# Kernel tuning notes

Measured on AMD Instinct MI355X. Metric: run time of the kernel, lower is better.

The kernel has to match this reference:

```python
import jax, jax.numpy as jnp
import numpy as np

B, S, DIM = 2, 2048, 2048
H = 16
Q_LORA, KV_LORA = 512, 512
D_NOPE, D_ROPE, D_V = 128, 64, 128
D_QK = D_NOPE + D_ROPE  # 192
SCALE = D_QK ** -0.5
EPS = 1e-6


def rmsnorm(x, w):
    return x * jax.lax.rsqrt(jnp.mean(x * x, axis=-1, keepdims=True) + EPS) * w


def apply_rope(x, cos, sin):
    # x: [B, S, h, d] with d even; cos/sin: [S, d//2] (complex-pair rotation)
    xs = x.reshape(*x.shape[:-1], -1, 2)
    x0, x1 = xs[..., 0], xs[..., 1]
    c = cos[None, :, None, :]
    s = sin[None, :, None, :]
    out = jnp.stack([x0 * c - x1 * s, x0 * s + x1 * c], axis=-1)
    return out.reshape(x.shape)


def setup_inputs() -> dict:
    key = jax.random.key(0)
    ks = jax.random.split(key, 8)
    std = 0.02
    x = jax.random.normal(ks[0], (B, S, DIM), dtype=jnp.float32)
    wq_a_w = jax.random.normal(ks[1], (DIM, Q_LORA), dtype=jnp.float32) * std
    wq_a_b = jnp.zeros((Q_LORA,), dtype=jnp.float32)
    q_norm_w = jnp.ones((Q_LORA,), dtype=jnp.float32)
    wq_b_w = jax.random.normal(ks[2], (Q_LORA, H * D_QK), dtype=jnp.float32) * std
    wkv_a_w = jax.random.normal(ks[3], (DIM, KV_LORA + D_ROPE), dtype=jnp.float32) * std
    wkv_a_b = jnp.zeros((KV_LORA + D_ROPE,), dtype=jnp.float32)
    kv_norm_w = jnp.ones((KV_LORA,), dtype=jnp.float32)
    wkv_b_w = jax.random.normal(ks[4], (KV_LORA, H * (D_NOPE + D_V)), dtype=jnp.float32) * std
    wo_w = jax.random.normal(ks[5], (H * D_V, DIM), dtype=jnp.float32) * std
    # rotary table: freqs_cis[t, i] = exp(1j * t * 10000^{-2i/d})
    inv_freq = 1.0 / (10000.0 ** (np.arange(0, D_ROPE, 2, dtype=np.float32) / D_ROPE))
    t = np.arange(S, dtype=np.float32)
    ang = np.outer(t, inv_freq)  # [S, D_ROPE//2]
    freqs_cos = jnp.asarray(np.cos(ang), dtype=jnp.float32)
    freqs_sin = jnp.asarray(np.sin(ang), dtype=jnp.float32)
    # causal mask (prefill): 0 on/below diagonal, -1e9 above
    mask = jnp.where(jnp.arange(S)[:, None] >= jnp.arange(S)[None, :], 0.0, -1e9).astype(jnp.float32)
    return {"x": x, "wq_a_w": wq_a_w, "wq_a_b": wq_a_b, "q_norm_w": q_norm_w,
            "wq_b_w": wq_b_w, "wkv_a_w": wkv_a_w, "wkv_a_b": wkv_a_b,
            "kv_norm_w": kv_norm_w, "wkv_b_w": wkv_b_w, "wo_w": wo_w,
            "freqs_cos": freqs_cos, "freqs_sin": freqs_sin, "mask": mask,
            "start_pos": 0}


def reference(x, wq_a_w, wq_a_b, q_norm_w, wq_b_w, wkv_a_w, wkv_a_b,
              kv_norm_w, wkv_b_w, wo_w, freqs_cos, freqs_sin, mask, start_pos):
    bsz, seqlen, _ = x.shape
    # low-rank Q: wq_b(q_norm(wq_a(x)))
    q = rmsnorm(x @ wq_a_w + wq_a_b, q_norm_w) @ wq_b_w
    q = q.reshape(bsz, seqlen, H, D_QK)
    q_nope, q_pe = q[..., :D_NOPE], q[..., D_NOPE:]
    q_pe = apply_rope(q_pe, freqs_cos, freqs_sin)
    # low-rank KV
    kv_full = x @ wkv_a_w + wkv_a_b
    kv, k_pe = kv_full[..., :KV_LORA], kv_full[..., KV_LORA:]
    k_pe = apply_rope(k_pe[:, :, None, :], freqs_cos, freqs_sin)  # [B,S,1,D_ROPE]
    kv = rmsnorm(kv, kv_norm_w) @ wkv_b_w
    kv = kv.reshape(bsz, seqlen, H, D_NOPE + D_V)
    k_nope, v = kv[..., :D_NOPE], kv[..., D_NOPE:]
    k = jnp.concatenate([k_nope, jnp.broadcast_to(k_pe, (bsz, seqlen, H, D_ROPE))], axis=-1)
    # prefill (start_pos=0): cache[:, :end_pos] == freshly written k, v
    q = jnp.concatenate([q_nope, q_pe], axis=-1)
    scores = jnp.einsum('bshd,bthd->bsht', q, k) * SCALE
    scores = scores + mask[None, :, None, :]
    attn = jax.nn.softmax(scores.astype(jnp.float32), axis=-1).astype(q.dtype)
    out = jnp.einsum('bsht,bthd->bshd', attn, v)
    return out.reshape(bsz, seqlen, H * D_V) @ wo_w
```

## Files before the change

### kernel.cpp

```cpp
#include <hip/hip_runtime.h>
#include <hip/hip_bf16.h>

typedef unsigned short u16;
typedef unsigned int u32;
typedef __attribute__((ext_vector_type(8))) __bf16 bf16x8;
typedef __attribute__((ext_vector_type(4))) float f32x4;
typedef __attribute__((ext_vector_type(4))) u32 u32x4;
typedef __attribute__((ext_vector_type(2))) u32 u32x2;

#define S_LEN 2048
#define BF16_ONE 0x3F80u

__device__ __forceinline__ float b2f(u16 u) {
  union { unsigned u; float f; } v; v.u = ((unsigned)u) << 16; return v.f;
}
__device__ __forceinline__ u16 f2b(float f) {
  union { float f; unsigned u; } v; v.f = f;
  unsigned r = v.u + 0x7fffu + ((v.u >> 16) & 1u);
  return (u16)(r >> 16);
}
__device__ __forceinline__ u32 cvt_pk_bf16(float a, float b) {
  u32 r;
  asm("v_cvt_pk_bf16_f32 %0, %1, %2" : "=v"(r) : "v"(a), "v"(b));
  return r;
}

__device__ __forceinline__ void glds16(const u16* g, u16* l) {
  __builtin_amdgcn_global_load_lds((const __attribute__((address_space(1))) void*)g,
                                   (__attribute__((address_space(3))) void*)l, 16, 0, 0);
}

__device__ __forceinline__ bool probe_f32(const u16* p) { return p[0] != (u16)BF16_ONE; }

struct CvtDesc {
  const void* src[7];
  u16* dst[7];
  int cum[8];
};
struct TrDesc {
  const void* in[5];
  u16* out[5];
  int R[5], C[5];
  int tcum[6];
  float scale[5];
};

__global__ __launch_bounds__(256) void prep_all(CvtDesc d, TrDesc td,
                                                const u16* __restrict__ probe,
                                                int cvt_total, int cvt_blocks) {
  const int tid = threadIdx.x;
  if ((int)blockIdx.x < cvt_blocks) {
    int i = blockIdx.x * 256 + tid;
    if (i >= cvt_total) return;
    int t = 0;
#pragma unroll
    for (int k = 1; k < 7; ++k) t += (i >= d.cum[k]);
    int li = i - d.cum[t];
    if (probe_f32(probe)) {
      const float* s = (const float*)d.src[t] + (long)li * 8;
      u16 tmp[8];
#pragma unroll
      for (int j = 0; j < 8; ++j) tmp[j] = f2b(s[j]);
      *(u32x4*)(d.dst[t] + (long)li * 8) = *(const u32x4*)tmp;
    } else {
      *(u32x4*)(d.dst[t] + (long)li * 8) = ((const u32x4*)d.src[t])[li];
    }
  } else {
    __shared__ u16 tile[32][33];
    int bid = blockIdx.x - cvt_blocks;
    int t = 0;
#pragma unroll
    for (int k = 1; k < 5; ++k) t += (bid >= td.tcum[k]);
    int rem = bid - td.tcum[t];
    const int R = td.R[t], C = td.C[t];
    const int tilesX = C >> 5;
    const int bx = rem % tilesX, by = rem / tilesX;
    const int c0 = bx * 32, r0 = by * 32;
    const int tx = tid & 31, ty = tid >> 5;
    const float sc = td.scale[t];
    if (probe_f32(probe)) {
      const float* inf = (const float*)td.in[t];
#pragma unroll
      for (int i = 0; i < 4; ++i)
        tile[ty + i * 8][tx] = f2b(inf[(long)(r0 + ty + i * 8) * C + c0 + tx] * sc);
    } else {
      const u16* inb = (const u16*)td.in[t];
#pragma unroll
      for (int i = 0; i < 4; ++i)
        tile[ty + i * 8][tx] = f2b(b2f(inb[(long)(r0 + ty + i * 8) * C + c0 + tx]) * sc);
    }
    __syncthreads();
    u16* outp = td.out[t];
#pragma unroll
    for (int i = 0; i < 4; ++i)
      outp[(long)(c0 + ty + i * 8) * R + r0 + tx] = tile[tx][ty + i * 8];
  }
}

template <int MT>
__global__ __launch_bounds__(256) void gemm_bt(const u16* __restrict__ A,
                                               const u16* __restrict__ Bt,
                                               const u16* __restrict__ bias,
                                               void* __restrict__ Cv,
                                               int M, int N, int K,
                                               const u16* __restrict__ oprobe,
                                               u16* __restrict__ vtOut) {
  constexpr int MI = MT / 32;
  __shared__ u16 As[2][MT * 32];
  __shared__ u16 Bs[2][128 * 32];
  const int tid = threadIdx.x;
  const int lane = tid & 63;
  const int w = tid >> 6;
  const int quad = lane >> 4;
  const int l16 = lane & 15;
  const int m0 = blockIdx.y * MT;
  const int n0 = blockIdx.x * 128;
  const int wm = (w >> 1) * (MT / 2);
  const int wn = (w & 1) * 64;

  const f32x4 zero = {0.f, 0.f, 0.f, 0.f};
  f32x4 acc[MI][4];
#pragma unroll
  for (int i = 0; i < MI; ++i)
#pragma unroll
    for (int j = 0; j < 4; ++j) acc[i][j] = zero;

  auto stage = [&](int k0, int buf) {
#pragma unroll
    for (int cc = 0; cc < MT * 4; cc += 256) {
      int j = cc + tid, ar = j >> 2, ak = ((j & 3) ^ (ar & 3)) * 8;
      glds16(A + (long)(m0 + ar) * K + k0 + ak, As[buf] + j * 8);
    }
#pragma unroll
    for (int cc = 0; cc < 512; cc += 256) {
      int j = cc + tid, br = j >> 2, bk = ((j & 3) ^ (br & 3)) * 8;
      int bn = n0 + br; if (bn > N - 1) bn = N - 1;
      glds16(Bt + (long)bn * K + k0 + bk, Bs[buf] + j * 8);
    }
  };

  const int nk = K >> 5;
  stage(0, 0);
  for (int t = 0; t < nk; ++t) {
    __syncthreads();
    if (t + 1 < nk) stage((t + 1) << 5, (t + 1) & 1);
    const u16* as = As[t & 1];
    const u16* bs = Bs[t & 1];
    bf16x8 af[MI], bfr[4];
#pragma unroll
    for (int mi = 0; mi < MI; ++mi)
      af[mi] = *(const bf16x8*)(as + (wm + mi * 16 + l16) * 32 +
                                ((quad ^ (l16 & 3)) * 8));
#pragma unroll
    for (int ni = 0; ni < 4; ++ni)
      bfr[ni] = *(const bf16x8*)(bs + (wn + ni * 16 + l16) * 32 +
                                 ((quad ^ (l16 & 3)) * 8));
#pragma unroll
    for (int mi = 0; mi < MI; ++mi)
#pragma unroll
      for (int ni = 0; ni < 4; ++ni)
        acc[mi][ni] = __builtin_amdgcn_mfma_f32_16x16x32_bf16(af[mi], bfr[ni],
                                                              acc[mi][ni], 0, 0, 0);
  }

  u16* C = (u16*)Cv;
  float* Cf = (float*)Cv;
  const bool of32 = oprobe && probe_f32(oprobe);
#pragma unroll
  for (int ni = 0; ni < 4; ++ni) {
    int col = n0 + wn + ni * 16 + l16;
    if (col >= N) continue;
    float bv = bias ? b2f(bias[col]) : 0.0f;
    const int lc = col & 255;
    const bool toV = (vtOut != nullptr) && (lc >= 128);
#pragma unroll
    for (int mi = 0; mi < MI; ++mi) {
      int row = m0 + wm + mi * 16 + quad * 4;
      if (toV) {
        int hh = col >> 8, d = lc - 128;
        int bb = row >> 11, s = row & 2047;
        u32 lo = (u32)f2b(acc[mi][ni][0] + bv) | ((u32)f2b(acc[mi][ni][1] + bv) << 16);
        u32 hi = (u32)f2b(acc[mi][ni][2] + bv) | ((u32)f2b(acc[mi][ni][3] + bv) << 16);
        u32x2 pk = {lo, hi};
        *(u32x2*)(vtOut + ((long)(bb * 16 + hh) * 128 + d) * 2048 + s) = pk;
      } else {
#pragma unroll
        for (int r = 0; r < 4; ++r) {
          float val = acc[mi][ni][r] + bv;
          if (of32) Cf[(long)(row + r) * N + col] = val;
          else      C[(long)(row + r) * N + col] = f2b(val);
        }
      }
    }
  }
}

__global__ __launch_bounds__(256) void gemm_qkv(const u16* __restrict__ qa,
                                                const u16* __restrict__ wqbT,
                                                u16* __restrict__ qbuf,
                                                const u16* __restrict__ kvn,
                                                const u16* __restrict__ wkvbT,
                                                u16* __restrict__ kvb,
                                                u16* __restrict__ vtb) {
  constexpr int MT = 128, MI = 4, K = 512;
  __shared__ u16 As[2][MT * 32];
  __shared__ u16 Bs[2][128 * 32];
  const bool isQ = blockIdx.x < 24;
  const u16* A  = isQ ? qa : kvn;
  const u16* Bt = isQ ? wqbT : wkvbT;
  u16* C        = isQ ? qbuf : kvb;
  u16* vtOut    = isQ ? (u16*)nullptr : vtb;
  const int N   = isQ ? 3072 : 4096;
  const int bx  = isQ ? (int)blockIdx.x : (int)blockIdx.x - 24;
  const int tid = threadIdx.x;
  const int lane = tid & 63;
  const int w = tid >> 6;
  const int quad = lane >> 4;
  const int l16 = lane & 15;
  const int m0 = blockIdx.y * MT;
  const int n0 = bx * 128;
  const int wm = (w >> 1) * (MT / 2);
  const int wn = (w & 1) * 64;

  const f32x4 zero = {0.f, 0.f, 0.f, 0.f};
  f32x4 acc[MI][4];
#pragma unroll
  for (int i = 0; i < MI; ++i)
#pragma unroll
    for (int j = 0; j < 4; ++j) acc[i][j] = zero;

  auto stage = [&](int k0, int buf) {
#pragma unroll
    for (int cc = 0; cc < MT * 4; cc += 256) {
      int j = cc + tid, ar = j >> 2, ak = ((j & 3) ^ (ar & 3)) * 8;
      glds16(A + (long)(m0 + ar) * K + k0 + ak, As[buf] + j * 8);
    }
#pragma unroll
    for (int cc = 0; cc < 512; cc += 256) {
      int j = cc + tid, br = j >> 2, bk = ((j & 3) ^ (br & 3)) * 8;
      glds16(Bt + (long)(n0 + br) * K + k0 + bk, Bs[buf] + j * 8);
    }
  };

  const int nk = K >> 5;
  stage(0, 0);
  for (int t = 0; t < nk; ++t) {
    __syncthreads();
    if (t + 1 < nk) stage((t + 1) << 5, (t + 1) & 1);
    const u16* as = As[t & 1];
    const u16* bs = Bs[t & 1];
    bf16x8 af[MI], bfr[4];
#pragma unroll
    for (int mi = 0; mi < MI; ++mi)
      af[mi] = *(const bf16x8*)(as + (wm + mi * 16 + l16) * 32 +
                                ((quad ^ (l16 & 3)) * 8));
#pragma unroll
    for (int ni = 0; ni < 4; ++ni)
      bfr[ni] = *(const bf16x8*)(bs + (wn + ni * 16 + l16) * 32 +
                                 ((quad ^ (l16 & 3)) * 8));
#pragma unroll
    for (int mi = 0; mi < MI; ++mi)
#pragma unroll
      for (int ni = 0; ni < 4; ++ni)
        acc[mi][ni] = __builtin_amdgcn_mfma_f32_16x16x32_bf16(af[mi], bfr[ni],
                                                              acc[mi][ni], 0, 0, 0);
  }

#pragma unroll
  for (int ni = 0; ni < 4; ++ni) {
    int col = n0 + wn + ni * 16 + l16;
    const int lc = col & 255;
    const bool toV = (vtOut != nullptr) && (lc >= 128);
#pragma unroll
    for (int mi = 0; mi < MI; ++mi) {
      int row = m0 + wm + mi * 16 + quad * 4;
      if (toV) {
        int hh = col >> 8, d = lc - 128;
        int bb = row >> 11, s = row & 2047;
        u32 lo = (u32)f2b(acc[mi][ni][0]) | ((u32)f2b(acc[mi][ni][1]) << 16);
        u32 hi = (u32)f2b(acc[mi][ni][2]) | ((u32)f2b(acc[mi][ni][3]) << 16);
        u32x2 pk = {lo, hi};
        *(u32x2*)(vtOut + ((long)(bb * 16 + hh) * 128 + d) * 2048 + s) = pk;
      } else {
#pragma unroll
        for (int r = 0; r < 4; ++r)
          C[(long)(row + r) * N + col] = f2b(acc[mi][ni][r]);
      }
    }
  }
}

__global__ __launch_bounds__(256) void rmsnorm_dual(const u16* __restrict__ qkva,
                                                    const u16* __restrict__ qw,
                                                    const u16* __restrict__ kw,
                                                    u16* __restrict__ qa,
                                                    u16* __restrict__ kvn) {
  __shared__ float red[4];
  const int bid = blockIdx.x;
  const bool kv = bid >= 4096;
  const int row = kv ? bid - 4096 : bid;
  const int tid = threadIdx.x;
  const u16* x = qkva + (long)row * 1088 + (kv ? 512 : 0);
  const u16* w = kv ? kw : qw;
  u16* y = (kv ? kvn : qa) + (long)row * 512;
  float v0 = b2f(x[tid]), v1 = b2f(x[tid + 256]);
  float ss = v0 * v0 + v1 * v1;
#pragma unroll
  for (int off = 1; off < 64; off <<= 1) ss += __shfl_xor(ss, off);
  if ((tid & 63) == 0) red[tid >> 6] = ss;
  __syncthreads();
  float tot = red[0] + red[1] + red[2] + red[3];
  float r = rsqrtf(tot * (1.0f / 512.0f) + 1e-6f);
  y[tid] = f2b(v0 * r * b2f(w[tid]));
  y[tid + 256] = f2b(v1 * r * b2f(w[tid + 256]));
}

__global__ __launch_bounds__(256) void rope_all(u16* __restrict__ q,
                                                const u16* __restrict__ qkva,
                                                u16* __restrict__ kpe,
                                                const u16* __restrict__ fc,
                                                const u16* __restrict__ fs) {
  const int bid = blockIdx.x;
  if (bid < 8192) {
    int i = bid * 256 + threadIdx.x;
    int pair = i & 31;
    int h = (i >> 5) & 15;
    int row = i >> 9;
    int pos = row & (S_LEN - 1);
    long base = (long)row * 3072 + h * 192 + 128 + pair * 2;
    float x0 = b2f(q[base]), x1 = b2f(q[base + 1]);
    float c = b2f(fc[pos * 32 + pair]), s = b2f(fs[pos * 32 + pair]);
    q[base] = f2b(x0 * c - x1 * s);
    q[base + 1] = f2b(x0 * s + x1 * c);
  } else {
    int i = (bid - 8192) * 256 + threadIdx.x;
    int pair = i & 31;
    int row = i >> 5;
    int pos = row & (S_LEN - 1);
    long sb = (long)row * 1088 + 1024 + pair * 2;
    float x0 = b2f(qkva[sb]), x1 = b2f(qkva[sb + 1]);
    float c = b2f(fc[pos * 32 + pair]), s = b2f(fs[pos * 32 + pair]);
    kpe[(long)row * 64 + pair * 2] = f2b(x0 * c - x1 * s);
    kpe[(long)row * 64 + pair * 2 + 1] = f2b(x0 * s + x1 * c);
  }
}

__global__ __launch_bounds__(512, 1) void mla_attn(const u16* __restrict__ q,
                                                   const u16* __restrict__ kvb,
                                                   const u16* __restrict__ vt,
                                                   const u16* __restrict__ kpe,
                                                   u16* __restrict__ o) {
  __shared__ u16 Ks[2][2][64 * 192];
  __shared__ u16 Vts[2][128 * 64];
  const int tid = threadIdx.x;
  const int w = tid >> 6;
  const int g = w >> 2;
  const int sw = w & 3;
  const int lane = tid & 63;
  const int quad = lane >> 4;
  const int l16 = lane & 15;
  const int bh = blockIdx.x;
  const int b = bh >> 4, h = bh & 15;
  const long rowbase = (long)b * S_LEN;
  const f32x4 zero = {0.f, 0.f, 0.f, 0.f};

  auto stage_k = [&](int t0s, u16* dst) {
#pragma unroll
    for (int tt = 0; tt < 3; ++tt) {
      int j = tt * 512 + tid;
      int r = j / 24, csw = j % 24;
      int c = csw ^ (r & 7);
      const u16* src = (c < 16)
                           ? (kvb + (rowbase + t0s + r) * 4096 + h * 256 + c * 8)
                           : (kpe + (rowbase + t0s + r) * 64 + (c - 16) * 8);
      glds16(src, dst + j * 8);
    }
  };
  auto stage_v = [&](int t0s, u16* dst) {
#pragma unroll
    for (int tt = 0; tt < 2; ++tt) {
      int j = tt * 512 + tid;
      int d = j >> 3, c = (j & 7) ^ (d & 7);
      glds16(vt + ((long)bh * 128 + d) * S_LEN + t0s + c * 8, dst + j * 8);
    }
  };

  const int srcA = (((quad & 1) << 1) | (quad >> 1)) * 16 + l16;
  const int srcB = srcA ^ 16;
  const bool lowq = quad < 2;
  const int p = quad & 1;

  const int yy = blockIdx.y;
  const int jt = (yy < 8) ? yy : 23 - yy;
  const int q0 = jt * 128;
  const int ns = jt + 1;
  const int rowlo = q0 + sw * 32;

  const u16* qrowA = q + (rowbase + rowlo + l16) * 3072 + h * 192;
  const u16* qrowB = qrowA + 16 * 3072;
  bf16x8 qfA[6], qfB[6];
#pragma unroll
  for (int kk = 0; kk < 6; ++kk) {
    qfA[kk] = *(const bf16x8*)(qrowA + kk * 32 + quad * 8);
    qfB[kk] = *(const bf16x8*)(qrowB + kk * 32 + quad * 8);
  }

  float mA = -INFINITY, mB = -INFINITY;
  float lA = 0.f, lB = 0.f;
  f32x4 oA[8], oB[8];
#pragma unroll
  for (int i = 0; i < 8; ++i) { oA[i] = zero; oB[i] = zero; }

  auto finish_half = [&](f32x4* s, float& m_r, float& l_r, f32x4* oacc,
                         int lim, bool needmask, bf16x8& ap0, bf16x8& ap1) {
    if (needmask) {
#pragma unroll
      for (int gg = 0; gg < 4; ++gg)
#pragma unroll
        for (int r = 0; r < 4; ++r)
          s[gg][r] = (gg * 16 + r > lim) ? -1e30f : s[gg][r];
    }
    float mx0 = fmaxf(fmaxf(s[0][0], s[0][1]), fmaxf(s[0][2], s[0][3]));
    float mx1 = fmaxf(fmaxf(s[1][0], s[1][1]), fmaxf(s[1][2], s[1][3]));
    float mx2 = fmaxf(fmaxf(s[2][0], s[2][1]), fmaxf(s[2][2], s[2][3]));
    float mx3 = fmaxf(fmaxf(s[3][0], s[3][1]), fmaxf(s[3][2], s[3][3]));
    float vmax = fmaxf(fmaxf(mx0, mx1), fmaxf(mx2, mx3));
    vmax = fmaxf(vmax, __shfl_xor(vmax, 16));
    vmax = fmaxf(vmax, __shfl_xor(vmax, 32));

    if (!__all(vmax <= m_r + 8.0f)) {
      float mnew = fmaxf(m_r, vmax);
      float alpha = __expf(m_r - mnew);
      m_r = mnew;
      l_r *= alpha;
      float al0 = __shfl(alpha, (lane & 48) | (quad * 4 + 0));
      float al1 = __shfl(alpha, (lane & 48) | (quad * 4 + 1));
      float al2 = __shfl(alpha, (lane & 48) | (quad * 4 + 2));
      float al3 = __shfl(alpha, (lane & 48) | (quad * 4 + 3));
#pragma unroll
      for (int nt = 0; nt < 8; ++nt) {
        f32x4 tt = oacc[nt];
        tt[0] *= al0; tt[1] *= al1; tt[2] *= al2; tt[3] *= al3;
        oacc[nt] = tt;
      }
    }

    float e00 = __expf(s[0][0] - m_r), e01 = __expf(s[0][1] - m_r);
    float e02 = __expf(s[0][2] - m_r), e03 = __expf(s[0][3] - m_r);
    float e10 = __expf(s[1][0] - m_r), e11 = __expf(s[1][1] - m_r);
    float e12 = __expf(s[1][2] - m_r), e13 = __expf(s[1][3] - m_r);
    float e20 = __expf(s[2][0] - m_r), e21 = __expf(s[2][1] - m_r);
    float e22 = __expf(s[2][2] - m_r), e23 = __expf(s[2][3] - m_r);
    float e30 = __expf(s[3][0] - m_r), e31 = __expf(s[3][1] - m_r);
    float e32 = __expf(s[3][2] - m_r), e33 = __expf(s[3][3] - m_r);
    l_r += ((e00 + e01) + (e02 + e03)) + ((e10 + e11) + (e12 + e13)) +
           ((e20 + e21) + (e22 + e23)) + ((e30 + e31) + (e32 + e33));
    u32 pk0x = cvt_pk_bf16(e00, e01), pk0y = cvt_pk_bf16(e02, e03);
    u32 pk1x = cvt_pk_bf16(e10, e11), pk1y = cvt_pk_bf16(e12, e13);
    u32 pk2x = cvt_pk_bf16(e20, e21), pk2y = cvt_pk_bf16(e22, e23);
    u32 pk3x = cvt_pk_bf16(e30, e31), pk3y = cvt_pk_bf16(e32, e33);

    u32 a0c = p ? pk1x : pk0x, a1c = p ? pk1y : pk0y;
    u32 a2c = p ? pk3x : pk2x, a3c = p ? pk3y : pk2y;
    u32 b0c = p ? pk0x : pk1x, b1c = p ? pk0y : pk1y;
    u32 b2c = p ? pk2x : pk3x, b3c = p ? pk2y : pk3y;
    u32 A0 = __shfl(a0c, srcA), A1 = __shfl(a1c, srcA);
    u32 A2 = __shfl(a2c, srcA), A3 = __shfl(a3c, srcA);
    u32 B0 = __shfl(b0c, srcB), B1 = __shfl(b1c, srcB);
    u32 B2 = __shfl(b2c, srcB), B3 = __shfl(b3c, srcB);
    u32x4 w0 = {lowq ? A0 : B0, lowq ? A1 : B1, lowq ? B0 : A0, lowq ? B1 : A1};
    u32x4 w1 = {lowq ? A2 : B2, lowq ? A3 : B3, lowq ? B2 : A2, lowq ? B3 : A3};
    ap0 = __builtin_bit_cast(bf16x8, w0);
    ap1 = __builtin_bit_cast(bf16x8, w1);
  };

  stage_k(0, Ks[0][0]);
  stage_k(64, Ks[0][1]);

  for (int i = 0; i < ns; ++i) {
    __syncthreads();
    stage_v((2 * i) * 64, Vts[0]);
    stage_v((2 * i + 1) * 64, Vts[1]);
    if (i + 1 < ns) {
      stage_k((2 * i + 2) * 64, Ks[(i + 1) & 1][0]);
      stage_k((2 * i + 3) * 64, Ks[(i + 1) & 1][1]);
    }
    const int t0 = (2 * i + g) * 64;
    const bool active = (rowlo + 31 >= t0);
    bf16x8 apA0, apA1, apB0, apB1;
    if (active) {
      const u16* ks = Ks[i & 1][g];
      f32x4 sA[4] = {zero, zero, zero, zero};
      f32x4 sB[4] = {zero, zero, zero, zero};
      __builtin_amdgcn_s_setprio(1);
#pragma unroll
      for (int kk = 0; kk < 6; ++kk) {
        const int csw = ((kk * 4 + quad) ^ (l16 & 7)) * 8;
#pragma unroll
        for (int gg = 0; gg < 4; ++gg) {
          bf16x8 kf = *(const bf16x8*)(ks + (gg * 16 + l16) * 192 + csw);
          sA[gg] = __builtin_amdgcn_mfma_f32_16x16x32_bf16(kf, qfA[kk], sA[gg], 0, 0, 0);
          sB[gg] = __builtin_amdgcn_mfma_f32_16x16x32_bf16(kf, qfB[kk], sB[gg], 0, 0, 0);
        }
      }
      __builtin_amdgcn_s_setprio(0);

      const bool nmA = (t0 + 63 > rowlo);
      const bool nmB = (t0 + 63 > rowlo + 16);
      const int limA = rowlo + l16 - t0 - quad * 4;
      finish_half(sA, mA, lA, oA, limA, nmA, apA0, apA1);
      finish_half(sB, mB, lB, oB, limA + 16, nmB, apB0, apB1);
    }
    __syncthreads();
    if (active) {
      const u16* vs = Vts[g];
      __builtin_amdgcn_s_setprio(1);
#pragma unroll
      for (int nt = 0; nt < 8; ++nt) {
        bf16x8 bv0 = *(const bf16x8*)(vs + (nt * 16 + l16) * 64 +
                                      ((quad ^ (l16 & 7)) * 8));
        bf16x8 bv1 = *(const bf16x8*)(vs + (nt * 16 + l16) * 64 +
                                      (((4 + quad) ^ (l16 & 7)) * 8));
        oA[nt] = __builtin_amdgcn_mfma_f32_16x16x32_bf16(apA0, bv0, oA[nt], 0, 0, 0);
        oA[nt] = __builtin_amdgcn_mfma_f32_16x16x32_bf16(apA1, bv1, oA[nt], 0, 0, 0);
        oB[nt] = __builtin_amdgcn_mfma_f32_16x16x32_bf16(apB0, bv0, oB[nt], 0, 0, 0);
        oB[nt] = __builtin_amdgcn_mfma_f32_16x16x32_bf16(apB1, bv1, oB[nt], 0, 0, 0);
      }
      __builtin_amdgcn_s_setprio(0);
    }
  }

  float lsA = lA; lsA += __shfl_xor(lsA, 16); lsA += __shfl_xor(lsA, 32);
  float lsB = lB; lsB += __shfl_xor(lsB, 16); lsB += __shfl_xor(lsB, 32);

  float* zone = (float*)&Ks[0][0][0];
  float* mlz = zone + 16384;
  if (g == 1) {
    float* zp0 = zone + ((sw * 2 + 0) * 64 + lane) * 32;
    float* zp1 = zone + ((sw * 2 + 1) * 64 + lane) * 32;
#pragma unroll
    for (int nt = 0; nt < 8; ++nt) {
      *(f32x4*)(zp0 + ((nt ^ (lane & 7)) << 2)) = oA[nt];
      *(f32x4*)(zp1 + ((nt ^ (lane & 7)) << 2)) = oB[nt];
    }
    mlz[((sw * 2 + 0) * 64 + lane) * 2 + 0] = mA;
    mlz[((sw * 2 + 0) * 64 + lane) * 2 + 1] = lsA;
    mlz[((sw * 2 + 1) * 64 + lane) * 2 + 0] = mB;
    mlz[((sw * 2 + 1) * 64 + lane) * 2 + 1] = lsB;
  }
  __syncthreads();
  if (g == 0) {
    auto merge_write = [&](float m_r, float ls, f32x4* oacc, int hz) {
      const float* zp = zone + ((sw * 2 + hz) * 64 + lane) * 32;
      float mo = mlz[((sw * 2 + hz) * 64 + lane) * 2 + 0];
      float lo = mlz[((sw * 2 + hz) * 64 + lane) * 2 + 1];
      float mm = fmaxf(m_r, mo);
      float aA = __expf(m_r - mm);
      float aB = __expf(mo - mm);
      float lt = ls * aA + lo * aB;
      float sAl = __fdividef(aA, lt);
      float sBl = __fdividef(aB, lt);
      float sa[4], sb[4];
#pragma unroll
      for (int r = 0; r < 4; ++r) {
        int src = (lane & 48) | (quad * 4 + r);
        sa[r] = __shfl(sAl, src);
        sb[r] = __shfl(sBl, src);
      }
      const long orow = rowbase + q0 + sw * 32 + hz * 16 + quad * 4;
#pragma unroll
      for (int nt = 0; nt < 8; ++nt) {
        f32x4 op = *(const f32x4*)(zp + ((nt ^ (lane & 7)) << 2));
#pragma unroll
        for (int r = 0; r < 4; ++r)
          o[(orow + r) * 2048 + h * 128 + nt * 16 + l16] =
              f2b(oacc[nt][r] * sa[r] + op[r] * sb[r]);
      }
    };
    merge_write(mA, lsA, oA, 0);
    merge_write(mB, lsB, oB, 1);
  }
}

extern "C" void kernel_launch(void* const* d_in, const int* in_sizes, int n_in,
                              void* d_out, int out_size, void* d_ws, size_t ws_size,
                              hipStream_t stream) {
  const void* x_raw    = d_in[0];
  const void* wqa_raw  = d_in[1];
  const void* wqab_raw = d_in[2];
  const void* qnw_raw  = d_in[3];
  const void* wqb_raw  = d_in[4];
  const void* wkva_raw = d_in[5];
  const void* wkvab_raw= d_in[6];
  const void* kvnw_raw = d_in[7];
  const void* wkvb_raw = d_in[8];
  const void* wo_raw   = d_in[9];
  const void* fc_raw   = d_in[10];
  const void* fs_raw   = d_in[11];
  const u16* probe = (const u16*)qnw_raw;
  const float SC = 0.07216878364870323f;

  char* ws = (char*)d_ws;
  size_t off = 0;
  auto alloc = [&](size_t n) { void* p = ws + off; off += (n + 255) & ~(size_t)255; return p; };
  u16* xb     = (u16*)alloc(4096ull * 2048 * 2);
  u16* fcb    = (u16*)alloc(2048ull * 32 * 2);
  u16* fsb    = (u16*)alloc(2048ull * 32 * 2);
  u16* biasc  = (u16*)alloc(1088ull * 2);
  u16* qnw_b  = (u16*)alloc(512ull * 2);
  u16* kvnw_b = (u16*)alloc(512ull * 2);
  u16* qkvat  = (u16*)alloc(1088ull * 2048 * 2);
  u16* wqb_t  = (u16*)alloc(3072ull * 512 * 2);
  u16* wkvb_t = (u16*)alloc(4096ull * 512 * 2);
  u16* wo_t   = (u16*)alloc(2048ull * 2048 * 2);
  u16* qkva   = (u16*)alloc(4096ull * 1088 * 2);
  u16* qa     = (u16*)alloc(4096ull * 512 * 2);
  u16* qbuf   = (u16*)alloc(4096ull * 3072 * 2);
  u16* kvn    = (u16*)alloc(4096ull * 512 * 2);
  u16* kpe    = (u16*)alloc(4096ull * 64 * 2);
  u16* kvb    = (u16*)alloc(4096ull * 4096 * 2);
  u16* vtb    = (u16*)alloc(32ull * 128 * 2048 * 2);
  u16* attn   = (u16*)alloc(4096ull * 2048 * 2);

  CvtDesc cd;
  const void* csrc[7] = {x_raw, fc_raw, fs_raw, wqab_raw, qnw_raw, wkvab_raw, kvnw_raw};
  u16* cdst[7] = {xb, fcb, fsb, biasc, qnw_b, biasc + 512, kvnw_b};
  long cn[7] = {4096l * 2048, 2048l * 32, 2048l * 32, 512, 512, 576, 512};
  int cum = 0;
  for (int i = 0; i < 7; ++i) {
    cd.src[i] = csrc[i]; cd.dst[i] = cdst[i];
    cd.cum[i] = cum; cum += (int)(cn[i] / 8);
  }
  cd.cum[7] = cum;

  TrDesc td;
  const void* tin[5] = {wqa_raw, wqb_raw, wkva_raw, wkvb_raw, wo_raw};
  u16* tout[5] = {qkvat, wqb_t, qkvat + 512ull * 2048, wkvb_t, wo_t};
  int tR[5] = {2048, 512, 2048, 512, 2048};
  int tC[5] = {512, 3072, 576, 4096, 2048};
  float tsc[5] = {1.0f, SC, 1.0f, 1.0f, 1.0f};
  int tcum = 0;
  for (int i = 0; i < 5; ++i) {
    td.in[i] = tin[i]; td.out[i] = tout[i];
    td.R[i] = tR[i]; td.C[i] = tC[i]; td.scale[i] = tsc[i];
    td.tcum[i] = tcum; tcum += (tR[i] / 32) * (tC[i] / 32);
  }
  td.tcum[5] = tcum;

  int cvt_blocks = (cum + 255) / 256;
  prep_all<<<cvt_blocks + tcum, 256, 0, stream>>>(cd, td, probe, cum, cvt_blocks);

  gemm_bt<128><<<dim3(9, 32), 256, 0, stream>>>(xb, qkvat, biasc, qkva, 4096, 1088, 2048,
                                                nullptr, nullptr);

  rmsnorm_dual<<<8192, 256, 0, stream>>>(qkva, qnw_b, kvnw_b, qa, kvn);

  gemm_qkv<<<dim3(56, 32), 256, 0, stream>>>(qa, wqb_t, qbuf, kvn, wkvb_t, kvb, vtb);

  rope_all<<<8704, 256, 0, stream>>>(qbuf, qkva, kpe, fcb, fsb);

  mla_attn<<<dim3(32, 16), 512, 0, stream>>>(qbuf, kvb, vtb, kpe, attn);

  gemm_bt<128><<<dim3(16, 32), 256, 0, stream>>>(attn, wo_t, nullptr, d_out, 4096, 2048, 2048,
                                                 probe, nullptr);
}
```

Before: 376.5 us.

## Fuse k_pe rope into rmsnorm kernel and apply q rope inside attention

Removes the standalone rope kernel. The k_pe rotation now runs in extra blocks of the rmsnorm kernel, and the q_pe rotation is applied to the Q fragments after they are loaded into registers in the attention kernel. This drops one launch and a full read-modify-write pass over the q buffer, in exchange for a few extra global loads of cos/sin and some ALU work at the start of each attention block. The pair mapping per lane has to match the fragment layout exactly.

Measured after the change: 373.6 us. About the same (-0.8%).

```diff
diff --git a/kernel.cpp b/kernel.cpp
--- a/kernel.cpp
+++ b/kernel.cpp
@@ -290,50 +290,18 @@
   }
 }
 
-__global__ __launch_bounds__(256) void rmsnorm_dual(const u16* __restrict__ qkva,
+__global__ __launch_bounds__(256) void rmsnorm_rope(const u16* __restrict__ qkva,
                                                     const u16* __restrict__ qw,
                                                     const u16* __restrict__ kw,
                                                     u16* __restrict__ qa,
-                                                    u16* __restrict__ kvn) {
-  __shared__ float red[4];
+                                                    u16* __restrict__ kvn,
+                                                    u16* __restrict__ kpe,
+                                                    const u16* __restrict__ fc,
+                                                    const u16* __restrict__ fs) {
   const int bid = blockIdx.x;
-  const bool kv = bid >= 4096;
-  const int row = kv ? bid - 4096 : bid;
   const int tid = threadIdx.x;
-  const u16* x = qkva + (long)row * 1088 + (kv ? 512 : 0);
-  const u16* w = kv ? kw : qw;
-  u16* y = (kv ? kvn : qa) + (long)row * 512;
-  float v0 = b2f(x[tid]), v1 = b2f(x[tid + 256]);
-  float ss = v0 * v0 + v1 * v1;
-#pragma unroll
-  for (int off = 1; off < 64; off <<= 1) ss += __shfl_xor(ss, off);
-  if ((tid & 63) == 0) red[tid >> 6] = ss;
-  __syncthreads();
-  float tot = red[0] + red[1] + red[2] + red[3];
-  float r = rsqrtf(tot * (1.0f / 512.0f) + 1e-6f);
-  y[tid] = f2b(v0 * r * b2f(w[tid]));
-  y[tid + 256] = f2b(v1 * r * b2f(w[tid + 256]));
-}
-
-__global__ __launch_bounds__(256) void rope_all(u16* __restrict__ q,
-                                                const u16* __restrict__ qkva,
-                                                u16* __restrict__ kpe,
-                                                const u16* __restrict__ fc,
-                                                const u16* __restrict__ fs) {
-  const int bid = blockIdx.x;
-  if (bid < 8192) {
-    int i = bid * 256 + threadIdx.x;
-    int pair = i & 31;
-    int h = (i >> 5) & 15;
-    int row = i >> 9;
-    int pos = row & (S_LEN - 1);
-    long base = (long)row * 3072 + h * 192 + 128 + pair * 2;
-    float x0 = b2f(q[base]), x1 = b2f(q[base + 1]);
-    float c = b2f(fc[pos * 32 + pair]), s = b2f(fs[pos * 32 + pair]);
-    q[base] = f2b(x0 * c - x1 * s);
-    q[base + 1] = f2b(x0 * s + x1 * c);
-  } else {
-    int i = (bid - 8192) * 256 + threadIdx.x;
+  if (bid >= 8192) {
+    int i = (bid - 8192) * 256 + tid;
     int pair = i & 31;
     int row = i >> 5;
     int pos = row & (S_LEN - 1);
@@ -342,13 +310,32 @@
     float c = b2f(fc[pos * 32 + pair]), s = b2f(fs[pos * 32 + pair]);
     kpe[(long)row * 64 + pair * 2] = f2b(x0 * c - x1 * s);
     kpe[(long)row * 64 + pair * 2 + 1] = f2b(x0 * s + x1 * c);
-  }
+    return;
+  }
+  __shared__ float red[4];
+  const bool kv = bid >= 4096;
+  const int row = kv ? bid - 4096 : bid;
+  const u16* x = qkva + (long)row * 1088 + (kv ? 512 : 0);
+  const u16* w = kv ? kw : qw;
+  u16* y = (kv ? kvn : qa) + (long)row * 512;
+  float v0 = b2f(x[tid]), v1 = b2f(x[tid + 256]);
+  float ss = v0 * v0 + v1 * v1;
+#pragma unroll
+  for (int off = 1; off < 64; off <<= 1) ss += __shfl_xor(ss, off);
+  if ((tid & 63) == 0) red[tid >> 6] = ss;
+  __syncthreads();
+  float tot = red[0] + red[1] + red[2] + red[3];
+  float r = rsqrtf(tot * (1.0f / 512.0f) + 1e-6f);
+  y[tid] = f2b(v0 * r * b2f(w[tid]));
+  y[tid + 256] = f2b(v1 * r * b2f(w[tid + 256]));
 }
 
 __global__ __launch_bounds__(512, 1) void mla_attn(const u16* __restrict__ q,
                                                    const u16* __restrict__ kvb,
                                                    const u16* __restrict__ vt,
                                                    const u16* __restrict__ kpe,
+                                                   const u16* __restrict__ fc,
+                                                   const u16* __restrict__ fs,
                                                    u16* __restrict__ o) {
   __shared__ u16 Ks[2][2][64 * 192];
   __shared__ u16 Vts[2][128 * 64];
@@ -403,6 +390,23 @@
   for (int kk = 0; kk < 6; ++kk) {
     qfA[kk] = *(const bf16x8*)(qrowA + kk * 32 + quad * 8);
     qfB[kk] = *(const bf16x8*)(qrowB + kk * 32 + quad * 8);
+  }
+  auto rope_frag = [&](bf16x8& f, int pos, int pb) {
+    u32x4 v = __builtin_bit_cast(u32x4, f);
+#pragma unroll
+    for (int j = 0; j < 4; ++j) {
+      u32 wv = v[j];
+      float x0 = b2f((u16)(wv & 0xffff)), x1 = b2f((u16)(wv >> 16));
+      float c = b2f(fc[pos * 32 + pb + j]), s = b2f(fs[pos * 32 + pb + j]);
+      v[j] = (u32)f2b(x0 * c - x1 * s) | ((u32)f2b(x0 * s + x1 * c) << 16);
+    }
+    f = __builtin_bit_cast(bf16x8, v);
+  };
+#pragma unroll
+  for (int kk = 4; kk < 6; ++kk) {
+    const int pb = (kk - 4) * 16 + quad * 4;
+    rope_frag(qfA[kk], rowlo + l16, pb);
+    rope_frag(qfB[kk], rowlo + 16 + l16, pb);
   }
 
   float mA = -INFINITY, mB = -INFINITY;
@@ -653,13 +657,11 @@
   gemm_bt<128><<<dim3(9, 32), 256, 0, stream>>>(xb, qkvat, biasc, qkva, 4096, 1088, 2048,
                                                 nullptr, nullptr);
 
-  rmsnorm_dual<<<8192, 256, 0, stream>>>(qkva, qnw_b, kvnw_b, qa, kvn);
+  rmsnorm_rope<<<8704, 256, 0, stream>>>(qkva, qnw_b, kvnw_b, qa, kvn, kpe, fcb, fsb);
 
   gemm_qkv<<<dim3(56, 32), 256, 0, stream>>>(qa, wqb_t, qbuf, kvn, wkvb_t, kvb, vtb);
 
-  rope_all<<<8704, 256, 0, stream>>>(qbuf, qkva, kpe, fcb, fsb);
-
-  mla_attn<<<dim3(32, 16), 512, 0, stream>>>(qbuf, kvb, vtb, kpe, attn);
+  mla_attn<<<dim3(32, 16), 512, 0, stream>>>(qbuf, kvb, vtb, kpe, fcb, fsb, attn);
 
   gemm_bt<128><<<dim3(16, 32), 256, 0, stream>>>(attn, wo_t, nullptr, d_out, 4096, 2048, 2048,
                                                  probe, nullptr);
```
